# Kernel optimization log

Measured on AMD Instinct MI355X. Metric: run time of the kernel, lower is better.

Reference implementation:

```python
import jax, jax.numpy as jnp
import numpy as np

T, B, D, H = 512, 64, 512, 1024


def setup_inputs() -> dict:
    key = jax.random.key(0)
    ks = jax.random.split(key, 4)
    scale = 1.0 / np.sqrt(D + H)
    return {
        "x": jax.random.normal(ks[0], (T, B, D), dtype=jnp.float32),
        "h0": jnp.zeros((B, H), dtype=jnp.float32),
        "Wz": jax.random.normal(ks[1], (H, D + H), dtype=jnp.float32) * scale,
        "bz": jnp.zeros((H,), dtype=jnp.float32),
        "Wr": jax.random.normal(ks[2], (H, D + H), dtype=jnp.float32) * scale,
        "br": jnp.zeros((H,), dtype=jnp.float32),
        "Wc": jax.random.normal(ks[3], (H, D + H), dtype=jnp.float32) * scale,
        "bc": jnp.zeros((H,), dtype=jnp.float32),
    }


def reference(x, h0, Wz, bz, Wr, br, Wc, bc):
    # x: [T, B, D], h0: [B, H]; weights follow torch Linear layout [out, in].
    def step(h, xt):
        xh = jnp.concatenate([xt, h], axis=-1)           # [B, D+H]
        z = jax.nn.sigmoid(xh @ Wz.T + bz)               # update gate [B, H]
        r = jax.nn.sigmoid(xh @ Wr.T + br)               # reset gate  [B, H]
        xrh = jnp.concatenate([xt, r * h], axis=-1)      # [B, D+H]
        hcand = jnp.tanh(xrh @ Wc.T + bc)                # candidate   [B, H]
        h_new = (1.0 - z) * h + z * hcand
        return h_new, h_new

    _, hist = jax.lax.scan(step, h0, x)                  # hist: [T, B, H]
    return hist
```

## Files before the change

### kernel.cpp

```cpp
#include <hip/hip_runtime.h>
#include <hip/hip_bf16.h>


typedef __attribute__((ext_vector_type(8))) short bf16x8;
typedef __attribute__((ext_vector_type(4))) float f32x4;

#define NWG 128
#define TSTEPS 512

#define AT_LD(p) __hip_atomic_load((p), __ATOMIC_RELAXED, __HIP_MEMORY_SCOPE_AGENT)

static __device__ __forceinline__ float sigmoidf_fast(float x) {
    return 1.0f / (1.0f + __expf(-x));
}

static __device__ __forceinline__ unsigned short float_to_bf16bits(float f) {
    __hip_bfloat16 b = __float2bfloat16(f);
    unsigned short us;
    __builtin_memcpy(&us, &b, 2);
    return us;
}

static __device__ __forceinline__ void store_coh_u16(void* p, unsigned short v) {
    unsigned vv = v;
    asm volatile("global_store_short %0, %1, off sc0 sc1"
                 :: "v"(p), "v"(vv) : "memory");
}
static __device__ __forceinline__ void store_coh_u32(unsigned* p, unsigned v) {
    asm volatile("global_store_dword %0, %1, off sc0 sc1"
                 :: "v"(p), "v"(v) : "memory");
}

__global__ __launch_bounds__(256) void k_convert_weights(
    const float* __restrict__ Wz, const float* __restrict__ Wr,
    const float* __restrict__ Wc,
    __hip_bfloat16* __restrict__ Wzr, __hip_bfloat16* __restrict__ Wcb)
{
    const long long NW = 1024LL * 1536LL;
    const long long stride = (long long)gridDim.x * blockDim.x;
    for (long long i = (long long)blockIdx.x * blockDim.x + threadIdx.x;
         i < 3 * NW; i += stride) {
        if (i < NW)            Wzr[i] = __float2bfloat16(Wz[i]);
        else if (i < 2 * NW)   Wzr[i] = __float2bfloat16(Wr[i - NW]);
        else                   Wcb[i - 2 * NW] = __float2bfloat16(Wc[i - 2 * NW]);
    }
}

__global__ __launch_bounds__(256) void k_convert_x(
    const float* __restrict__ x, __hip_bfloat16* __restrict__ xb)
{
    const long long N = 512LL * 64LL * 512LL;
    const long long stride = (long long)gridDim.x * blockDim.x;
    for (long long i = (long long)blockIdx.x * blockDim.x + threadIdx.x;
         i < N; i += stride)
        xb[i] = __float2bfloat16(x[i]);
}

__global__ __launch_bounds__(256) void k_init_h(
    const float* __restrict__ h0, __hip_bfloat16* __restrict__ hb)
{
    int i = blockIdx.x * blockDim.x + threadIdx.x;
    hb[i] = __float2bfloat16(h0[i]);
}

__global__ __launch_bounds__(256, 1) void k_gru_persistent(
    const __hip_bfloat16* __restrict__ xb,
    const float* __restrict__ h0,
    __hip_bfloat16* __restrict__ hb_,
    const __hip_bfloat16* __restrict__ Wzr,
    const __hip_bfloat16* __restrict__ Wcb,
    const float* __restrict__ bz, const float* __restrict__ br,
    const float* __restrict__ bc,
    __hip_bfloat16* __restrict__ sb_,
    float* __restrict__ out,
    unsigned* __restrict__ flags)
{
    __shared__ short w1z[64 * 16 * 8];
    __shared__ short w1r[64 * 16 * 8];
    __shared__ short w2c[64 * 16 * 8];
    __shared__ f32x4 red[2][2][64];

    short* hb = (short*)hb_;
    short* sb = (short*)sb_;

    const int g = blockIdx.x;
    const int lane = threadIdx.x & 63;
    const int wave = threadIdx.x >> 6;
    const int r15 = lane & 15;
    const int q = lane >> 4;
    const int kk = q << 3;

    const int dom = g & 1;
    const int wgid = g >> 1;
    const int c0 = wgid * 16;
    const int B0 = dom * 32;
    const int tile = wave & 1;
    const int kh = wave >> 1;
    const int mt = B0 + tile * 16;
    const int jcol = c0 + r15;
    const int mb = mt + (q << 2);
    const bool owner = (wave < 2);

    unsigned* myline = flags + (dom * 64 + wgid) * 32;
    const unsigned* pollflag = flags + (dom * 64 + lane) * 32;

    for (int c = threadIdx.x; c < 64 * 16; c += 256) {
        int row = c & 15, blk = c >> 4;
        bf16x8 vz = *(const bf16x8*)((const short*)Wzr +
                                     (long long)(c0 + row) * 1536 + blk * 8);
        bf16x8 vr = *(const bf16x8*)((const short*)Wzr +
                                     (long long)(1024 + c0 + row) * 1536 + blk * 8);
        bf16x8 vc = *(const bf16x8*)((const short*)Wcb +
                                     (long long)(c0 + row) * 1536 + blk * 8);
        *(bf16x8*)(w1z + c * 8) = vz;
        *(bf16x8*)(w1r + c * 8) = vr;
        *(bf16x8*)(w2c + c * 8) = vc;
    }

    bf16x8 wzh[16], wrh[16], wcs[16];
#pragma unroll
    for (int i = 0; i < 16; ++i) {
        int bk = 64 + kh * 64 + i * 4 + q;
        wzh[i] = *(const bf16x8*)((const short*)Wzr +
                                  (long long)(c0 + r15) * 1536 + bk * 8);
        wrh[i] = *(const bf16x8*)((const short*)Wzr +
                                  (long long)(1024 + c0 + r15) * 1536 + bk * 8);
        wcs[i] = *(const bf16x8*)((const short*)Wcb +
                                  (long long)(c0 + r15) * 1536 + bk * 8);
    }

    const float biasZ = bz[jcol];
    const float biasR = br[jcol];
    const float biasC = bc[jcol];

    float hreg[4];
    if (owner) {
#pragma unroll
        for (int v = 0; v < 4; ++v)
            hreg[v] = h0[(mb + v) * 1024 + jcol];
    }
    __syncthreads();

    float zreg[4] = {0.f, 0.f, 0.f, 0.f};

    bf16x8 xc[8];
    {
        const short* Ax0 = (const short*)xb + (mt + r15) * 512 + kh * 256 + kk;
#pragma unroll
        for (int i = 0; i < 8; ++i)
            xc[i] = *(const bf16x8*)(Ax0 + i * 32);
    }

    for (int t = 0; t < TSTEPS; ++t) {
        unsigned f1;
        asm volatile("global_load_dword %0, %1, off sc0 sc1"
                     : "=&v"(f1) : "v"(pollflag) : "memory");

        f32x4 zA = {0.f,0.f,0.f,0.f}, zB = {0.f,0.f,0.f,0.f};
        f32x4 rA = {0.f,0.f,0.f,0.f}, rB = {0.f,0.f,0.f,0.f};
#pragma unroll
        for (int i = 0; i < 8; ++i) {
            int bk = kh * 32 + i * 4 + q;
            bf16x8 wz = *(const bf16x8*)(w1z + (bk * 16 + r15) * 8);
            bf16x8 wr = *(const bf16x8*)(w1r + (bk * 16 + r15) * 8);
            if (i & 1) { zB = __builtin_amdgcn_mfma_f32_16x16x32_bf16(xc[i], wz, zB, 0, 0, 0);
                         rB = __builtin_amdgcn_mfma_f32_16x16x32_bf16(xc[i], wr, rB, 0, 0, 0); }
            else       { zA = __builtin_amdgcn_mfma_f32_16x16x32_bf16(xc[i], wz, zA, 0, 0, 0);
                         rA = __builtin_amdgcn_mfma_f32_16x16x32_bf16(xc[i], wr, rA, 0, 0, 0); }
        }
        asm volatile("s_waitcnt vmcnt(0)" ::: "memory");
        __builtin_amdgcn_sched_barrier(0);
        {
            const unsigned gen = (unsigned)(2 * t);
            if (!__all(f1 >= gen)) {
                bool ok;
                do {
                    __builtin_amdgcn_s_sleep(1);
                    unsigned fv;
                    asm volatile("global_load_dword %0, %1, off sc0 sc1\n\t"
                                 "s_waitcnt vmcnt(0)"
                                 : "=&v"(fv) : "v"(pollflag) : "memory");
                    ok = (fv >= gen);
                } while (__any(!ok));
            }
        }
        __builtin_amdgcn_sched_barrier(0);

        bf16x8 fr[16], xn[8];
        {
            const short* Ah = hb + (mt + r15) * 1024 + kh * 512 + kk;
            const int tn = (t + 1 < TSTEPS) ? t + 1 : t;
            const short* AxN = (const short*)xb + (long long)tn * 64 * 512 +
                               (mt + r15) * 512 + kh * 256 + kk;
#pragma unroll
            for (int i = 0; i < 16; ++i)
                asm volatile("global_load_dwordx4 %0, %1, off sc0 sc1"
                             : "=&v"(fr[i]) : "v"(Ah + i * 32));
#pragma unroll
            for (int i = 0; i < 8; ++i)
                asm volatile("global_load_dwordx4 %0, %1, off"
                             : "=&v"(xn[i]) : "v"(AxN + i * 32));
            asm volatile("s_waitcnt vmcnt(0)" ::: "memory");
            __builtin_amdgcn_sched_barrier(0);
        }
#pragma unroll
        for (int i = 0; i < 16; ++i) {
            if (i & 1) { zB = __builtin_amdgcn_mfma_f32_16x16x32_bf16(fr[i], wzh[i], zB, 0, 0, 0);
                         rB = __builtin_amdgcn_mfma_f32_16x16x32_bf16(fr[i], wrh[i], rB, 0, 0, 0); }
            else       { zA = __builtin_amdgcn_mfma_f32_16x16x32_bf16(fr[i], wzh[i], zA, 0, 0, 0);
                         rA = __builtin_amdgcn_mfma_f32_16x16x32_bf16(fr[i], wrh[i], rA, 0, 0, 0); }
        }
        {
            f32x4 pz = zA + zB;
            f32x4 pr = rA + rB;
            if (!owner) { red[tile][0][lane] = pz; red[tile][1][lane] = pr; }
            __syncthreads();
            if (owner) {
                f32x4 oz = red[tile][0][lane];
                f32x4 orr = red[tile][1][lane];
#pragma unroll
                for (int v = 0; v < 4; ++v) {
                    zreg[v] = sigmoidf_fast(pz[v] + oz[v] + biasZ);
                    float rv = sigmoidf_fast(pr[v] + orr[v] + biasR);
                    store_coh_u16(sb + (mb + v) * 1024 + jcol,
                                  float_to_bf16bits(rv * hreg[v]));
                }
            }
        }
        asm volatile("s_waitcnt vmcnt(0)" ::: "memory");
        __syncthreads();
        if (threadIdx.x == 0) store_coh_u32(myline, (unsigned)(2 * t + 1));

        unsigned f2;
        asm volatile("global_load_dword %0, %1, off sc0 sc1"
                     : "=&v"(f2) : "v"(pollflag) : "memory");

        f32x4 cA = {0.f,0.f,0.f,0.f}, cB = {0.f,0.f,0.f,0.f};
#pragma unroll
        for (int i = 0; i < 8; ++i) {
            int bk = kh * 32 + i * 4 + q;
            bf16x8 wc = *(const bf16x8*)(w2c + (bk * 16 + r15) * 8);
            if (i & 1) cB = __builtin_amdgcn_mfma_f32_16x16x32_bf16(xc[i], wc, cB, 0, 0, 0);
            else       cA = __builtin_amdgcn_mfma_f32_16x16x32_bf16(xc[i], wc, cA, 0, 0, 0);
        }
        asm volatile("s_waitcnt vmcnt(0)" ::: "memory");
        __builtin_amdgcn_sched_barrier(0);
        {
            const unsigned gen = (unsigned)(2 * t + 1);
            if (!__all(f2 >= gen)) {
                bool ok;
                do {
                    __builtin_amdgcn_s_sleep(1);
                    unsigned fv;
                    asm volatile("global_load_dword %0, %1, off sc0 sc1\n\t"
                                 "s_waitcnt vmcnt(0)"
                                 : "=&v"(fv) : "v"(pollflag) : "memory");
                    ok = (fv >= gen);
                } while (__any(!ok));
            }
        }
        __builtin_amdgcn_sched_barrier(0);

        {
            const short* As = sb + (mt + r15) * 1024 + kh * 512 + kk;
            bf16x8 fs[16];
#pragma unroll
            for (int i = 0; i < 16; ++i)
                asm volatile("global_load_dwordx4 %0, %1, off sc0 sc1"
                             : "=&v"(fs[i]) : "v"(As + i * 32));
            asm volatile("s_waitcnt vmcnt(0)" ::: "memory");
            __builtin_amdgcn_sched_barrier(0);
#pragma unroll
            for (int i = 0; i < 16; ++i) {
                if (i & 1) cB = __builtin_amdgcn_mfma_f32_16x16x32_bf16(fs[i], wcs[i], cB, 0, 0, 0);
                else       cA = __builtin_amdgcn_mfma_f32_16x16x32_bf16(fs[i], wcs[i], cA, 0, 0, 0);
            }
            f32x4 pc = cA + cB;
            if (!owner) red[tile][0][lane] = pc;
            __syncthreads();
            if (owner) {
                f32x4 oc = red[tile][0][lane];
#pragma unroll
                for (int v = 0; v < 4; ++v) {
                    float cv = tanhf(pc[v] + oc[v] + biasC);
                    float h_new = (1.0f - zreg[v]) * hreg[v] + zreg[v] * cv;
                    hreg[v] = h_new;
                    store_coh_u16(hb + (mb + v) * 1024 + jcol,
                                  float_to_bf16bits(h_new));
                }
            }
        }
        asm volatile("s_waitcnt vmcnt(0)" ::: "memory");
        __syncthreads();
        if (threadIdx.x == 0) store_coh_u32(myline, (unsigned)(2 * t + 2));

        if (owner) {
            float* outt = out + (long long)t * 64 * 1024;
#pragma unroll
            for (int v = 0; v < 4; ++v)
                outt[(mb + v) * 1024 + jcol] = hreg[v];
        }
#pragma unroll
        for (int i = 0; i < 8; ++i) xc[i] = xn[i];
    }
}

extern "C" void kernel_launch(void* const* d_in, const int* in_sizes, int n_in,
                              void* d_out, int out_size, void* d_ws, size_t ws_size,
                              hipStream_t stream)
{
    (void)in_sizes; (void)n_in; (void)out_size; (void)ws_size;
    const float* x  = (const float*)d_in[0];
    const float* h0 = (const float*)d_in[1];
    const float* Wz = (const float*)d_in[2];
    const float* bz = (const float*)d_in[3];
    const float* Wr = (const float*)d_in[4];
    const float* br = (const float*)d_in[5];
    const float* Wc = (const float*)d_in[6];
    const float* bc = (const float*)d_in[7];
    float* out = (float*)d_out;

    char* ws = (char*)d_ws;
    __hip_bfloat16* Wzr = (__hip_bfloat16*)(ws);
    __hip_bfloat16* Wcb = (__hip_bfloat16*)(ws + 6291456);
    __hip_bfloat16* xb  = (__hip_bfloat16*)(ws + 9437184);
    __hip_bfloat16* hb  = (__hip_bfloat16*)(ws + 42991616);
    __hip_bfloat16* sb  = (__hip_bfloat16*)(ws + 43122688);
    unsigned*    flags  = (unsigned*)(ws + 43253760);

    k_convert_weights<<<1024, 256, 0, stream>>>(Wz, Wr, Wc, Wzr, Wcb);
    k_convert_x<<<2048, 256, 0, stream>>>(x, xb);
    k_init_h<<<256, 256, 0, stream>>>(h0, hb);
    (void)hipMemsetAsync(flags, 0, 2 * 64 * 32 * sizeof(unsigned), stream);

    k_gru_persistent<<<NWG, 256, 0, stream>>>(
        xb, h0, hb, Wzr, Wcb, bz, br, bc, sb, out, flags);
}
```

Before: 4.839 ms.

## Repartition persistent GRU into 4 batch domains of 32 columns each

Changes the work split of the persistent kernel from 2 batch domains × 64 workgroups (16 hidden columns, 32 batch rows) to 4 domains × 32 workgroups (32 hidden columns, 16 batch rows), with the two tile waves now covering different column halves instead of different batch tiles. Each sync domain then has half as many participants to poll, which shortens the cross-workgroup barrier. The spin loops also drop s_sleep so waiters react faster, at the cost of more polling traffic. LDS weight slabs double in size, and the per-step weight reuse across batch rows drops.

```diff
diff --git a/kernel.cpp b/kernel.cpp
--- a/kernel.cpp
+++ b/kernel.cpp
@@ -7,8 +7,6 @@
 
 #define NWG 128
 #define TSTEPS 512
-
-#define AT_LD(p) __hip_atomic_load((p), __ATOMIC_RELAXED, __HIP_MEMORY_SCOPE_AGENT)
 
 static __device__ __forceinline__ float sigmoidf_fast(float x) {
     return 1.0f / (1.0f + __expf(-x));
@@ -75,9 +73,9 @@
     float* __restrict__ out,
     unsigned* __restrict__ flags)
 {
-    __shared__ short w1z[64 * 16 * 8];
-    __shared__ short w1r[64 * 16 * 8];
-    __shared__ short w2c[64 * 16 * 8];
+    __shared__ short w1z[64 * 32 * 8];
+    __shared__ short w1r[64 * 32 * 8];
+    __shared__ short w2c[64 * 32 * 8];
     __shared__ f32x4 red[2][2][64];
 
     short* hb = (short*)hb_;
@@ -90,31 +88,30 @@
     const int q = lane >> 4;
     const int kk = q << 3;
 
-    const int dom = g & 1;
-    const int wgid = g >> 1;
-    const int c0 = wgid * 16;
-    const int B0 = dom * 32;
+    const int dom = g & 3;
+    const int wgid = g >> 2;
+    const int c0 = wgid * 32;
+    const int mt = dom * 16;
     const int tile = wave & 1;
     const int kh = wave >> 1;
-    const int mt = B0 + tile * 16;
-    const int jcol = c0 + r15;
+    const int jcol = c0 + tile * 16 + r15;
     const int mb = mt + (q << 2);
-    const bool owner = (wave < 2);
-
-    unsigned* myline = flags + (dom * 64 + wgid) * 32;
-    const unsigned* pollflag = flags + (dom * 64 + lane) * 32;
-
-    for (int c = threadIdx.x; c < 64 * 16; c += 256) {
-        int row = c & 15, blk = c >> 4;
+    const bool owner = (kh == 0);
+
+    unsigned* myline = flags + (dom * 32 + wgid) * 32;
+    const unsigned* pollflag = flags + (dom * 32 + (lane & 31)) * 32;
+
+    for (int c = threadIdx.x; c < 64 * 32; c += 256) {
+        int row = c & 31, blk = c >> 5;
         bf16x8 vz = *(const bf16x8*)((const short*)Wzr +
                                      (long long)(c0 + row) * 1536 + blk * 8);
         bf16x8 vr = *(const bf16x8*)((const short*)Wzr +
                                      (long long)(1024 + c0 + row) * 1536 + blk * 8);
         bf16x8 vc = *(const bf16x8*)((const short*)Wcb +
                                      (long long)(c0 + row) * 1536 + blk * 8);
-        *(bf16x8*)(w1z + c * 8) = vz;
-        *(bf16x8*)(w1r + c * 8) = vr;
-        *(bf16x8*)(w2c + c * 8) = vc;
+        *(bf16x8*)(w1z + (blk * 32 + row) * 8) = vz;
+        *(bf16x8*)(w1r + (blk * 32 + row) * 8) = vr;
+        *(bf16x8*)(w2c + (blk * 32 + row) * 8) = vc;
     }
 
     bf16x8 wzh[16], wrh[16], wcs[16];
@@ -122,11 +119,11 @@
     for (int i = 0; i < 16; ++i) {
         int bk = 64 + kh * 64 + i * 4 + q;
         wzh[i] = *(const bf16x8*)((const short*)Wzr +
-                                  (long long)(c0 + r15) * 1536 + bk * 8);
+                                  (long long)jcol * 1536 + bk * 8);
         wrh[i] = *(const bf16x8*)((const short*)Wzr +
-                                  (long long)(1024 + c0 + r15) * 1536 + bk * 8);
+                                  (long long)(1024 + jcol) * 1536 + bk * 8);
         wcs[i] = *(const bf16x8*)((const short*)Wcb +
-                                  (long long)(c0 + r15) * 1536 + bk * 8);
+                                  (long long)jcol * 1536 + bk * 8);
     }
 
     const float biasZ = bz[jcol];
@@ -161,8 +158,8 @@
 #pragma unroll
         for (int i = 0; i < 8; ++i) {
             int bk = kh * 32 + i * 4 + q;
-            bf16x8 wz = *(const bf16x8*)(w1z + (bk * 16 + r15) * 8);
-            bf16x8 wr = *(const bf16x8*)(w1r + (bk * 16 + r15) * 8);
+            bf16x8 wz = *(const bf16x8*)(w1z + (bk * 32 + tile * 16 + r15) * 8);
+            bf16x8 wr = *(const bf16x8*)(w1r + (bk * 32 + tile * 16 + r15) * 8);
             if (i & 1) { zB = __builtin_amdgcn_mfma_f32_16x16x32_bf16(xc[i], wz, zB, 0, 0, 0);
                          rB = __builtin_amdgcn_mfma_f32_16x16x32_bf16(xc[i], wr, rB, 0, 0, 0); }
             else       { zA = __builtin_amdgcn_mfma_f32_16x16x32_bf16(xc[i], wz, zA, 0, 0, 0);
@@ -175,7 +172,6 @@
             if (!__all(f1 >= gen)) {
                 bool ok;
                 do {
-                    __builtin_amdgcn_s_sleep(1);
                     unsigned fv;
                     asm volatile("global_load_dword %0, %1, off sc0 sc1\n\t"
                                  "s_waitcnt vmcnt(0)"
@@ -239,7 +235,7 @@
 #pragma unroll
         for (int i = 0; i < 8; ++i) {
             int bk = kh * 32 + i * 4 + q;
-            bf16x8 wc = *(const bf16x8*)(w2c + (bk * 16 + r15) * 8);
+            bf16x8 wc = *(const bf16x8*)(w2c + (bk * 32 + tile * 16 + r15) * 8);
             if (i & 1) cB = __builtin_amdgcn_mfma_f32_16x16x32_bf16(xc[i], wc, cB, 0, 0, 0);
             else       cA = __builtin_amdgcn_mfma_f32_16x16x32_bf16(xc[i], wc, cA, 0, 0, 0);
         }
@@ -250,7 +246,6 @@
             if (!__all(f2 >= gen)) {
                 bool ok;
                 do {
-                    __builtin_amdgcn_s_sleep(1);
                     unsigned fv;
                     asm volatile("global_load_dword %0, %1, off sc0 sc1\n\t"
                                  "s_waitcnt vmcnt(0)"
@@ -331,7 +326,7 @@
     k_convert_weights<<<1024, 256, 0, stream>>>(Wz, Wr, Wc, Wzr, Wcb);
     k_convert_x<<<2048, 256, 0, stream>>>(x, xb);
     k_init_h<<<256, 256, 0, stream>>>(h0, hb);
-    (void)hipMemsetAsync(flags, 0, 2 * 64 * 32 * sizeof(unsigned), stream);
+    (void)hipMemsetAsync(flags, 0, 4 * 32 * 32 * sizeof(unsigned), stream);
 
     k_gru_persistent<<<NWG, 256, 0, stream>>>(
         xb, h0, hb, Wzr, Wcb, bz, br, bc, sb, out, flags);
```

New measurement: 4.285 ms. 11.5% less time.
